# Performance work log

Hardware: AMD Instinct MI355X
Metric: run time of the kernel (lower is better)

Reference implementation:

```python
import jax, jax.numpy as jnp
import numpy as np

BETA = 0.25  # args.beta
B, T, D, K = 16, 4096, 64, 1024


def setup_inputs() -> dict:
    key = jax.random.key(0)
    kz, kw = jax.random.split(key)
    z = jax.random.normal(kz, (B, T, D), dtype=jnp.float32)
    # nn.Embedding weight init: uniform(-1/K, 1/K)
    emb = jax.random.uniform(kw, (K, D), dtype=jnp.float32,
                             minval=-1.0 / K, maxval=1.0 / K)
    return {"z": z, "emb": emb}


def reference(z, emb):
    # z: [B, T, D] (torch code loops over first dim; all elements non-empty here)
    # emb: [K, D] codebook
    b, t, d = z.shape
    zf = z.reshape(-1, d)                                   # [B*T, D]
    # squared euclidean distances: ||z||^2 + ||e||^2 - 2 z.e
    dist = (jnp.sum(zf * zf, axis=1, keepdims=True)
            + jnp.sum(emb * emb, axis=1)
            - 2.0 * zf @ emb.T)                             # [B*T, K]
    idx = jnp.argmin(dist, axis=1).reshape(b, t)            # [B, T] int
    z_q_raw = emb[idx]                                      # [B, T, D] gather
    sg = jax.lax.stop_gradient
    # per-batch-element means, summed (loop accumulates loss per z_t)
    commit = jnp.mean((sg(z_q_raw) - z) ** 2, axis=(1, 2))  # [B]
    codebk = jnp.mean((z_q_raw - sg(z)) ** 2, axis=(1, 2))  # [B]
    loss = jnp.sum(BETA * commit + codebk)
    # straight-through estimator
    z_q = z + sg(z_q_raw - z)
    return z_q, loss, idx
```

## Files before the change

kernel.cpp:

```cpp
#include <hip/hip_runtime.h>
#include <math.h>
#include <float.h>

#define NROWS    65536
#define DD       64
#define KK       1024
#define LOSS_OFF 4194304
#define IDX_OFF  4194305
#define RPB      64
#define MAXC     32
#define TPR      4
#define NRND     16

typedef short  short8 __attribute__((ext_vector_type(8)));
typedef float  f32x4  __attribute__((ext_vector_type(4)));

__device__ __forceinline__ void async_copy16(void* lds, const void* g) {
    __builtin_amdgcn_global_load_lds(
        (const __attribute__((address_space(1))) unsigned int*)g,
        (__attribute__((address_space(3))) unsigned int*)lds, 16, 0, 0);
}

__device__ __forceinline__ unsigned short bf16rne(float x) {
    unsigned int u = __float_as_uint(x);
    return (unsigned short)((u + 0x7fffu + ((u >> 16) & 1u)) >> 16);
}

__device__ __forceinline__ float np_sumsq64_stream(const float* p) {
#pragma clang fp contract(off)
    float r[8];
    {
        const float4 u0 = *reinterpret_cast<const float4*>(p);
        const float4 u1 = *reinterpret_cast<const float4*>(p + 4);
        r[0] = u0.x * u0.x; r[1] = u0.y * u0.y; r[2] = u0.z * u0.z; r[3] = u0.w * u0.w;
        r[4] = u1.x * u1.x; r[5] = u1.y * u1.y; r[6] = u1.z * u1.z; r[7] = u1.w * u1.w;
    }
#pragma unroll
    for (int i = 8; i < 64; i += 8) {
        const float4 u0 = *reinterpret_cast<const float4*>(p + i);
        const float4 u1 = *reinterpret_cast<const float4*>(p + i + 4);
        r[0] += u0.x * u0.x; r[1] += u0.y * u0.y; r[2] += u0.z * u0.z; r[3] += u0.w * u0.w;
        r[4] += u1.x * u1.x; r[5] += u1.y * u1.y; r[6] += u1.z * u1.z; r[7] += u1.w * u1.w;
    }
    return ((r[0] + r[1]) + (r[2] + r[3])) + ((r[4] + r[5]) + (r[6] + r[7]));
}

__global__ void vq_prep(const float* __restrict__ emb,
                        float* __restrict__ bn,
                        unsigned short* __restrict__ ebf) {
#pragma clang fp contract(off)
    const int gtid = blockIdx.x * 256 + threadIdx.x;
    const int code = gtid >> 3;
    const int j    = gtid & 7;
    const float* ep = emb + (size_t)code * DD;
    float r = 0.f;
#pragma unroll
    for (int i = 0; i < 8; ++i) {
        const float v = ep[8 * i + j];
        r += v * v;
    }
    const float s1 = r  + __shfl_xor(r,  1, 64);
    const float s2 = s1 + __shfl_xor(s1, 2, 64);
    const float s3 = s2 + __shfl_xor(s2, 4, 64);
    if (j == 0) bn[code] = s3;

    const float* cp = emb + (size_t)gtid * 8;
    const float4 u0 = *reinterpret_cast<const float4*>(cp);
    const float4 u1 = *reinterpret_cast<const float4*>(cp + 4);
    short8 s;
    s[0] = (short)bf16rne(u0.x); s[1] = (short)bf16rne(u0.y);
    s[2] = (short)bf16rne(u0.z); s[3] = (short)bf16rne(u0.w);
    s[4] = (short)bf16rne(u1.x); s[5] = (short)bf16rne(u1.y);
    s[6] = (short)bf16rne(u1.z); s[7] = (short)bf16rne(u1.w);
    const int g    = code >> 4;
    const int c16s = code & 15;
    const int half = j >> 2;
    const int qq   = j & 3;
    const size_t doff = (size_t)g * 1024 + half * 512 + (qq * 16 + c16s) * 8;
    *reinterpret_cast<short8*>(ebf + doff) = s;
}

__global__ __launch_bounds__(256)
void vq_main(const float* __restrict__ z, const float* __restrict__ emb,
             const unsigned short* __restrict__ ebf,
             const float* __restrict__ bn, float* __restrict__ out) {
    __shared__ char  dbuf[2][TPR * 2048] __attribute__((aligned(16)));
    __shared__ float a_s[RPB];
    __shared__ float bn_s[KK];
    __shared__ int   cnt[RPB];
    __shared__ int   clist[RPB][MAXC];
    __shared__ int   bidx[RPB];

    const int tid  = threadIdx.x;
    const int lane = tid & 63;
    const int wv   = __builtin_amdgcn_readfirstlane(tid) >> 6;
    const int q    = lane >> 4;
    const int c16  = lane & 15;
    const int rowbase = blockIdx.x * RPB;

    const char* sbase = (const char*)ebf + (size_t)lane * 16;
    char* dst0 = &dbuf[0][wv * 2048 + lane * 16];
    char* dst1 = &dbuf[1][wv * 2048 + lane * 16];

    if (tid < RPB) {
        a_s[tid] = np_sumsq64_stream(z + (size_t)(rowbase + tid) * DD);
        cnt[tid] = 0;
    }
    {
        const int i = tid * 4;
        *reinterpret_cast<float4*>(&bn_s[i]) =
            *reinterpret_cast<const float4*>(bn + i);
    }

    short8 afr[2];
#pragma unroll
    for (int kh = 0; kh < 2; ++kh) {
        const float* zp = z + (size_t)(rowbase + 16 * wv + c16) * DD
                          + 32 * kh + 8 * q;
        const float4 u0 = *reinterpret_cast<const float4*>(zp);
        const float4 u1 = *reinterpret_cast<const float4*>(zp + 4);
        short8 s;
        s[0] = (short)bf16rne(u0.x); s[1] = (short)bf16rne(u0.y);
        s[2] = (short)bf16rne(u0.z); s[3] = (short)bf16rne(u0.w);
        s[4] = (short)bf16rne(u1.x); s[5] = (short)bf16rne(u1.y);
        s[6] = (short)bf16rne(u1.z); s[7] = (short)bf16rne(u1.w);
        afr[kh] = s;
    }

    auto stage = [&](int R, int buf) {
        const char* s0 = sbase + (size_t)(TPR * R + wv) * 2048;
        char* d = buf ? dst1 : dst0;
        async_copy16(d,        s0);
        async_copy16(d + 1024, s0 + 1024);
    };

    stage(0, 0);
    __syncthreads();

    float wadd[4];
#pragma unroll
    for (int i = 0; i < 4; ++i) {
        const int rowl = 16 * wv + 4 * q + i;
        wadd[i] = 1.8e-4f * sqrtf(a_s[rowl]) + 1.2e-4f;
    }

    float mn[4];
#pragma unroll
    for (int i = 0; i < 4; ++i) mn[i] = FLT_MAX;

    for (int R = 0; R < NRND; ++R) {
        const int cur = R & 1;
        if (R < NRND - 1) stage(R + 1, cur ^ 1);
        float dv[TPR][4];
#pragma unroll
        for (int j = 0; j < TPR; ++j) {
            const char* tb = &dbuf[cur][j * 2048 + lane * 16];
            const short8 b0 = *reinterpret_cast<const short8*>(tb);
            const short8 b1 = *reinterpret_cast<const short8*>(tb + 1024);
            f32x4 acc = {0.f, 0.f, 0.f, 0.f};
            acc = __builtin_amdgcn_mfma_f32_16x16x32_bf16(afr[0], b0, acc, 0, 0, 0);
            acc = __builtin_amdgcn_mfma_f32_16x16x32_bf16(afr[1], b1, acc, 0, 0, 0);
            const float bnv = bn_s[16 * (TPR * R + j) + c16];
#pragma unroll
            for (int r = 0; r < 4; ++r)
                dv[j][r] = fmaf(-2.f, acc[r], bnv);
        }
#pragma unroll
        for (int j = 0; j < TPR; ++j)
#pragma unroll
            for (int r = 0; r < 4; ++r)
                mn[r] = fminf(mn[r], dv[j][r]);
#pragma unroll
        for (int mask = 1; mask < 16; mask <<= 1)
#pragma unroll
            for (int r = 0; r < 4; ++r)
                mn[r] = fminf(mn[r], __shfl_xor(mn[r], mask, 64));
        float thr[4];
#pragma unroll
        for (int r = 0; r < 4; ++r) thr[r] = mn[r] + wadd[r];
#pragma unroll
        for (int j = 0; j < TPR; ++j) {
            const int col = 16 * (TPR * R + j) + c16;
#pragma unroll
            for (int r = 0; r < 4; ++r) {
                if (dv[j][r] <= thr[r]) {
                    const int rowl = 16 * wv + 4 * q + r;
                    const int slot = atomicAdd(&cnt[rowl], 1);
                    if (slot < MAXC) clist[rowl][slot] = col;
                }
            }
        }
        __syncthreads();
    }

    {
        const int rowl = 16 * wv + c16;
        const int row  = rowbase + rowl;
        const int nc   = cnt[rowl];
        const bool full = nc > MAXC;
        const int lim  = full ? KK : nc;
        const float av = a_s[rowl];
        const float* zp = z + (size_t)row * DD;
        float sb = FLT_MAX;
        int   cb = 0x7fffffff;
        for (int jj = q; jj < lim; jj += 4) {
            const int c = full ? jj : clist[rowl][jj];
            const float* ep = emb + (size_t)c * DD;
            float dot = 0.f;
#pragma unroll
            for (int d = 0; d < DD; d += 4) {
                const float4 zv = *reinterpret_cast<const float4*>(zp + d);
                const float4 ev = *reinterpret_cast<const float4*>(ep + d);
                dot = fmaf(zv.x, ev.x, dot); dot = fmaf(zv.y, ev.y, dot);
                dot = fmaf(zv.z, ev.z, dot); dot = fmaf(zv.w, ev.w, dot);
            }
            const float tt = av + bn_s[c];
            const float sd = fmaf(-2.f, dot, tt);
            if (sd < sb || (sd == sb && c < cb)) { sb = sd; cb = c; }
        }
#pragma unroll
        for (int mask = 16; mask < 64; mask <<= 1) {
            const float so = __shfl_xor(sb, mask, 64);
            const int   co = __shfl_xor(cb, mask, 64);
            if (so < sb || (so == sb && co < cb)) { sb = so; cb = co; }
        }
        if (cb > 1023) cb = 0;
        if (q == 0) bidx[rowl] = cb;
    }
    __syncthreads();

    if (tid >= RPB) return;
    const int row = rowbase + tid;
    const int bid = bidx[tid];
    const float* ep = emb + (size_t)bid * DD;
    const float* zp = z + (size_t)row * DD;
    float* op = out + (size_t)row * DD;
    double sac = 0.0;
#pragma unroll
    for (int d = 0; d < DD; d += 4) {
        const float4 zv = *reinterpret_cast<const float4*>(zp + d);
        const float4 e4 = *reinterpret_cast<const float4*>(ep + d);
        const float df0 = e4.x - zv.x;
        const float df1 = e4.y - zv.y;
        const float df2 = e4.z - zv.z;
        const float df3 = e4.w - zv.w;
        float4 qv;
        qv.x = zv.x + df0; qv.y = zv.y + df1;
        qv.z = zv.z + df2; qv.w = zv.w + df3;
        *reinterpret_cast<float4*>(op + d) = qv;
        sac += (double)(df0 * df0); sac += (double)(df1 * df1);
        sac += (double)(df2 * df2); sac += (double)(df3 * df3);
    }
    out[IDX_OFF + row] = (float)bid;

#pragma unroll
    for (int off = 32; off > 0; off >>= 1) sac += __shfl_down(sac, off, 64);
    if (lane == 0)
        atomicAdd(&out[LOSS_OFF], (float)((1.25 * sac) / 262144.0));
}

extern "C" void kernel_launch(void* const* d_in, const int* in_sizes, int n_in,
                              void* d_out, int out_size, void* d_ws, size_t ws_size,
                              hipStream_t stream) {
    const float* z   = (const float*)d_in[0];
    const float* emb = (const float*)d_in[1];
    float* out = (float*)d_out;

    float*          bnw = (float*)d_ws;
    unsigned short* ebf = (unsigned short*)((char*)d_ws + 4096);

    vq_prep<<<dim3(32), dim3(256), 0, stream>>>(emb, bnw, ebf);
    vq_main<<<dim3(NROWS / RPB), dim3(256), 0, stream>>>(z, emb, ebf, bnw, out);
}
```

Measured before the change: 127.1 us.

## Spread row norm and epilogue work across all four wavefronts

The per-row squared-norm prologue previously ran on one wavefront, with one thread serially reading a whole 64-float row. It now uses all 256 threads, 8 lanes per row with xor-shuffle reductions. The epilogue that writes z_q and accumulates the loss likewise moves from one wavefront with one thread per row to 4 threads per row handling 16 elements each. A block-level LDS reduction then issues one atomic per block. This targets the serialized prologue and epilogue latency, at the cost of an extra barrier and a changed summation order for the norms and the loss.

```diff
diff --git a/kernel.cpp b/kernel.cpp
--- a/kernel.cpp
+++ b/kernel.cpp
@@ -26,23 +26,15 @@
     return (unsigned short)((u + 0x7fffu + ((u >> 16) & 1u)) >> 16);
 }
 
-__device__ __forceinline__ float np_sumsq64_stream(const float* p) {
+__device__ __forceinline__ float np_acc8(const float* p, int j) {
 #pragma clang fp contract(off)
-    float r[8];
-    {
-        const float4 u0 = *reinterpret_cast<const float4*>(p);
-        const float4 u1 = *reinterpret_cast<const float4*>(p + 4);
-        r[0] = u0.x * u0.x; r[1] = u0.y * u0.y; r[2] = u0.z * u0.z; r[3] = u0.w * u0.w;
-        r[4] = u1.x * u1.x; r[5] = u1.y * u1.y; r[6] = u1.z * u1.z; r[7] = u1.w * u1.w;
-    }
-#pragma unroll
-    for (int i = 8; i < 64; i += 8) {
-        const float4 u0 = *reinterpret_cast<const float4*>(p + i);
-        const float4 u1 = *reinterpret_cast<const float4*>(p + i + 4);
-        r[0] += u0.x * u0.x; r[1] += u0.y * u0.y; r[2] += u0.z * u0.z; r[3] += u0.w * u0.w;
-        r[4] += u1.x * u1.x; r[5] += u1.y * u1.y; r[6] += u1.z * u1.z; r[7] += u1.w * u1.w;
-    }
-    return ((r[0] + r[1]) + (r[2] + r[3])) + ((r[4] + r[5]) + (r[6] + r[7]));
+    float r = 0.f;
+#pragma unroll
+    for (int i = 0; i < 8; ++i) {
+        const float v = p[8 * i + j];
+        r += v * v;
+    }
+    return r;
 }
 
 __global__ void vq_prep(const float* __restrict__ emb,
@@ -90,6 +82,7 @@
     __shared__ int   cnt[RPB];
     __shared__ int   clist[RPB][MAXC];
     __shared__ int   bidx[RPB];
+    __shared__ double lsum[4];
 
     const int tid  = threadIdx.x;
     const int lane = tid & 63;
@@ -102,10 +95,19 @@
     char* dst0 = &dbuf[0][wv * 2048 + lane * 16];
     char* dst1 = &dbuf[1][wv * 2048 + lane * 16];
 
-    if (tid < RPB) {
-        a_s[tid] = np_sumsq64_stream(z + (size_t)(rowbase + tid) * DD);
-        cnt[tid] = 0;
-    }
+    {
+        const int j8 = tid & 7;
+#pragma unroll
+        for (int sw = 0; sw < 2; ++sw) {
+            const int rowl = 32 * sw + (tid >> 3);
+            const float r = np_acc8(z + (size_t)(rowbase + rowl) * DD, j8);
+            const float s1 = r  + __shfl_xor(r,  1, 64);
+            const float s2 = s1 + __shfl_xor(s1, 2, 64);
+            const float s3 = s2 + __shfl_xor(s2, 4, 64);
+            if (j8 == 0) a_s[rowl] = s3;
+        }
+    }
+    if (tid < RPB) cnt[tid] = 0;
     {
         const int i = tid * 4;
         *reinterpret_cast<float4*>(&bn_s[i]) =
@@ -229,34 +231,44 @@
     }
     __syncthreads();
 
-    if (tid >= RPB) return;
-    const int row = rowbase + tid;
-    const int bid = bidx[tid];
-    const float* ep = emb + (size_t)bid * DD;
-    const float* zp = z + (size_t)row * DD;
-    float* op = out + (size_t)row * DD;
-    double sac = 0.0;
-#pragma unroll
-    for (int d = 0; d < DD; d += 4) {
-        const float4 zv = *reinterpret_cast<const float4*>(zp + d);
-        const float4 e4 = *reinterpret_cast<const float4*>(ep + d);
-        const float df0 = e4.x - zv.x;
-        const float df1 = e4.y - zv.y;
-        const float df2 = e4.z - zv.z;
-        const float df3 = e4.w - zv.w;
-        float4 qv;
-        qv.x = zv.x + df0; qv.y = zv.y + df1;
-        qv.z = zv.z + df2; qv.w = zv.w + df3;
-        *reinterpret_cast<float4*>(op + d) = qv;
-        sac += (double)(df0 * df0); sac += (double)(df1 * df1);
-        sac += (double)(df2 * df2); sac += (double)(df3 * df3);
-    }
-    out[IDX_OFF + row] = (float)bid;
-
-#pragma unroll
-    for (int off = 32; off > 0; off >>= 1) sac += __shfl_down(sac, off, 64);
-    if (lane == 0)
-        atomicAdd(&out[LOSS_OFF], (float)((1.25 * sac) / 262144.0));
+    {
+        const int rowl = tid >> 2;
+        const int sub  = tid & 3;
+        const int row  = rowbase + rowl;
+        const int bid  = bidx[rowl];
+        const float* ep = emb + (size_t)bid * DD + sub * 16;
+        const float* zp = z + (size_t)row * DD + sub * 16;
+        float* op = out + (size_t)row * DD + sub * 16;
+        double sac = 0.0;
+#pragma unroll
+        for (int d = 0; d < 16; d += 4) {
+            const float4 zv = *reinterpret_cast<const float4*>(zp + d);
+            const float4 e4 = *reinterpret_cast<const float4*>(ep + d);
+            const float df0 = e4.x - zv.x;
+            const float df1 = e4.y - zv.y;
+            const float df2 = e4.z - zv.z;
+            const float df3 = e4.w - zv.w;
+            float4 qv;
+            qv.x = zv.x + df0; qv.y = zv.y + df1;
+            qv.z = zv.z + df2; qv.w = zv.w + df3;
+            *reinterpret_cast<float4*>(op + d) = qv;
+            sac += (double)(df0 * df0); sac += (double)(df1 * df1);
+            sac += (double)(df2 * df2); sac += (double)(df3 * df3);
+        }
+        if (sub == 0) out[IDX_OFF + row] = (float)bid;
+
+        sac += __shfl_down(sac, 1, 64);
+        sac += __shfl_down(sac, 2, 64);
+        double v = (sub == 0) ? sac : 0.0;
+#pragma unroll
+        for (int off = 32; off > 0; off >>= 1) v += __shfl_down(v, off, 64);
+        if (lane == 0) lsum[wv] = v;
+    }
+    __syncthreads();
+    if (tid == 0)
+        atomicAdd(&out[LOSS_OFF],
+                  (float)((1.25 * (lsum[0] + lsum[1] + lsum[2] + lsum[3]))
+                          / 262144.0));
 }
 
 extern "C" void kernel_launch(void* const* d_in, const int* in_sizes, int n_in,
```

Result: no change. 125.3 us (-1.4%).
